# Performance work log

Hardware: AMD Instinct MI355X
Metric: run time of the kernel (lower is better)

## Reference

```python
import jax, jax.numpy as jnp
import numpy as np

H, W, C, B = 16, 16, 2048, 32
HEADS = 4
D1, D2 = 256, 128


def _build_edges(h, w):
    """Lattice + mirror + disease-node + self-loop edges (PyG GATConv default adds self loops)."""
    idx = lambda i, j: i * w + j
    edges = []
    for i in range(h):
        for j in range(w):
            if i + 1 < h:
                edges += [(idx(i, j), idx(i + 1, j)), (idx(i + 1, j), idx(i, j))]
            if j + 1 < w:
                edges += [(idx(i, j), idx(i, j + 1)), (idx(i, j + 1), idx(i, j))]
            mj = w - j - 1
            if mj != j:
                edges.append((idx(i, j), idx(i, mj)))
    n = h * w
    for i in range(n):  # disease node (index n), bidirectional
        edges += [(i, n), (n, i)]
    for i in range(n + 1):  # self loops
        edges.append((i, i))
    e = np.asarray(edges, dtype=np.int32)
    return jnp.asarray(e[:, 0]), jnp.asarray(e[:, 1])


def setup_inputs() -> dict:
    key = jax.random.key(0)
    ks = jax.random.split(key, 16)
    s = 0.02
    src, dst = _build_edges(H, W)
    return {
        "fmap": jax.random.normal(ks[0], (B, C, H, W), jnp.float32),
        "W1": jax.random.normal(ks[1], (C, HEADS * D1), jnp.float32) * s,
        "a_src1": jax.random.normal(ks[2], (HEADS, D1), jnp.float32) * s,
        "a_dst1": jax.random.normal(ks[3], (HEADS, D1), jnp.float32) * s,
        "b1": jnp.zeros((D1,), jnp.float32),
        "W2": jax.random.normal(ks[4], (D1, HEADS * D2), jnp.float32) * s,
        "a_src2": jax.random.normal(ks[5], (HEADS, D2), jnp.float32) * s,
        "a_dst2": jax.random.normal(ks[6], (HEADS, D2), jnp.float32) * s,
        "b2": jnp.zeros((D2,), jnp.float32),
        "Wp": jax.random.normal(ks[7], (D2, 1), jnp.float32) * s,
        "bp": jnp.zeros((1,), jnp.float32),
        "Wc1": jax.random.normal(ks[8], (D2, 64), jnp.float32) * s,
        "bc1": jnp.zeros((64,), jnp.float32),
        "Wc2": jax.random.normal(ks[9], (64, 1), jnp.float32) * s,
        "bc2": jnp.zeros((1,), jnp.float32),
        "src": src,
        "dst": dst,
    }


def _gat_layer(x, src, dst, Wm, a_s, a_d, b, heads, out_dim):
    """PyG GATConv math: concat=False (mean over heads), leaky_relu slope 0.2."""
    N = x.shape[0]
    h = (x @ Wm).reshape(N, heads, out_dim)           # [N, H, D]
    es = jnp.sum(h * a_s, axis=-1)                    # [N, H]
    ed = jnp.sum(h * a_d, axis=-1)                    # [N, H]
    e = jax.nn.leaky_relu(es[src] + ed[dst], 0.2)     # [E, H]
    m = jax.ops.segment_max(e, dst, num_segments=N)   # softmax over incoming edges
    alpha = jnp.exp(e - m[dst])
    denom = jax.ops.segment_sum(alpha, dst, num_segments=N)
    alpha = alpha / (denom[dst] + 1e-16)
    agg = jax.ops.segment_sum(alpha[:, :, None] * h[src], dst, num_segments=N)
    return agg.mean(axis=1) + b                       # [N, D]


def reference(fmap, W1, a_src1, a_dst1, b1, W2, a_src2, a_dst2, b2,
              Wp, bp, Wc1, bc1, Wc2, bc2, src, dst):
    Bn, Cc, Hh, Ww = fmap.shape
    nodes = fmap.reshape(Bn, Cc, Hh * Ww).transpose(0, 2, 1)   # [B, HW, C]
    nodes = jnp.concatenate([nodes, jnp.zeros((Bn, 1, Cc), nodes.dtype)], axis=1)

    def per_graph(x):
        x = _gat_layer(x, src, dst, W1, a_src1, a_dst1, b1, HEADS, D1)
        x = _gat_layer(x, src, dst, W2, a_src2, a_dst2, b2, HEADS, D2)
        w = jax.nn.sigmoid(x @ Wp + bp)               # [N, 1] attention pool weights
        g = jnp.mean(x * w, axis=0)                   # global_mean_pool, single graph
        h1 = jax.nn.relu(g @ Wc1 + bc1)
        pred = jax.nn.sigmoid(h1 @ Wc2 + bc2)         # [1]
        return pred[0], w[:, 0]

    preds, atts = jax.vmap(per_graph)(nodes)          # [B], [B, N]
    return preds, atts
```

## Files before the change

### kernel.cpp

```cpp
#include <hip/hip_runtime.h>

typedef __bf16 bf16_t;
typedef __bf16 bf16x8 __attribute__((ext_vector_type(8)));
typedef float f32x4 __attribute__((ext_vector_type(4)));

#define MPAD  8320
#define NNODE 257
#define NB    32

__device__ __forceinline__ void gld_lds16(const bf16_t* g, bf16_t* l) {
    __builtin_amdgcn_global_load_lds(
        (const __attribute__((address_space(1))) void*)g,
        (__attribute__((address_space(3))) void*)l, 16, 0, 0);
}

__global__ __launch_bounds__(256) void setup_kernel(const float* __restrict__ W1, bf16_t* __restrict__ W1t,
                                                    const float* __restrict__ W2, bf16_t* __restrict__ W2t,
                                                    const float* __restrict__ fmap, bf16_t* __restrict__ X,
                                                    const int* __restrict__ dstv, int E,
                                                    int* __restrict__ indptr, int* __restrict__ eidx,
                                                    float* __restrict__ zbase, bf16_t* __restrict__ out1) {
    __shared__ float smem[64 * 65];
    int idx = blockIdx.x, t = threadIdx.x;
    if (idx < 2176) {
        const float* W; bf16_t* Wt; int K, N, kt, nt;
        if (idx < 2048) { W = W1; Wt = W1t; K = 2048; N = 1024; kt = idx >> 5; nt = idx & 31; }
        else { int l = idx - 2048; W = W2; Wt = W2t; K = 256; N = 512; kt = l >> 4; nt = l & 15; }
        int k0 = kt * 32, n0 = nt * 32;
        int tx = t & 31, ty = t >> 5;
#pragma unroll
        for (int i = 0; i < 4; i++)
            smem[(ty + i * 8) * 33 + tx] = W[(size_t)(k0 + ty + i * 8) * N + n0 + tx];
        __syncthreads();
#pragma unroll
        for (int i = 0; i < 4; i++)
            Wt[(size_t)(n0 + ty + i * 8) * K + k0 + tx] = (bf16_t)smem[tx * 33 + ty + i * 8];
    } else if (idx < 6272) {
        int local = idx - 2176;
        int ct = local & 31, rem = local >> 5;
        int nt = rem & 3, b = rem >> 2;
        int c0 = ct * 64, n0 = nt * 64;
        const float* f = fmap + (size_t)b * 2048 * 256;
        int ln = t & 63, lc = t >> 6;
#pragma unroll
        for (int i = 0; i < 16; i++) {
            int c = lc + i * 4;
            smem[c * 65 + ln] = f[(size_t)(c0 + c) * 256 + n0 + ln];
        }
        __syncthreads();
        int sn = t >> 3, sc = (t & 7) * 8;
#pragma unroll
        for (int half = 0; half < 2; half++) {
            int n = sn + half * 32;
            bf16_t tmp[8];
#pragma unroll
            for (int j = 0; j < 8; j++) tmp[j] = (bf16_t)smem[(sc + j) * 65 + n];
            *(bf16x8*)&X[(size_t)(b * 257 + n0 + n) * 2048 + c0 + sc] = *(bf16x8*)tmp;
        }
    } else if (idx < 6402) {
        int local = idx - 6272;
        uint4* p = (uint4*)zbase + (size_t)local * 256;
        p[t] = uint4{0, 0, 0, 0};
    } else if (idx < 6530) {
        int i = idx - 6402;
        int row = (i < 32) ? (i * 257 + 256) : (8224 + (i - 32));
        uint4* p = (uint4*)(X + (size_t)row * 2048);
        p[t] = uint4{0, 0, 0, 0};
    } else if (idx < 6542) {
        int local = idx - 6530;
        uint4* p = (uint4*)((char*)(out1 + (size_t)8224 * 256) + (size_t)local * 4096);
        p[t] = uint4{0, 0, 0, 0};
    } else {
        __shared__ int cnt[258];
        __shared__ int off[258];
        for (int i = t; i < 258; i += 256) cnt[i] = 0;
        __syncthreads();
        for (int e = t; e < E; e += 256) atomicAdd(&cnt[dstv[e] + 1], 1);
        __syncthreads();
        if (t == 0) {
            int s = 0;
            for (int i = 0; i < 258; i++) { s += cnt[i]; off[i] = s; }
        }
        __syncthreads();
        for (int i = t; i < 258; i += 256) indptr[i] = off[i];
        __syncthreads();
        for (int e = t; e < E; e += 256) {
            int p = atomicAdd(&off[dstv[e]], 1);
            eidx[p] = e;
        }
    }
}

__global__ __launch_bounds__(128, 2) void gemm_kernel(const bf16_t* __restrict__ A,
                                                      const bf16_t* __restrict__ Bt,
                                                      bf16_t* __restrict__ C,
                                                      const float* __restrict__ asrc,
                                                      const float* __restrict__ adst,
                                                      float* __restrict__ es,
                                                      float* __restrict__ ed,
                                                      int K, int N, int headD) {
    __shared__ __align__(16) bf16_t sm[3 * 8192];
    int row0 = blockIdx.y * 128, col0 = blockIdx.x * 128;
    int t = threadIdx.x;
    int wave = t >> 6, lane = t & 63;
    int srow = lane >> 2, scol = (lane & 3) * 8;
    const bf16_t* Abase = A + (size_t)row0 * K;
    const bf16_t* Bbase = Bt + (size_t)col0 * K;
    f32x4 acc[4][8] = {};
    int fr = lane & 15;
    int kq = (lane >> 4) * 8;
    int nk = K >> 5;
    auto issue = [&](int kt, int stage) {
        bf16_t* As = sm + stage * 8192;
        bf16_t* Bs = As + 4096;
        int k0 = kt << 5;
#pragma unroll
        for (int c = 0; c < 4; c++) {
            int chunk = wave * 4 + c;
            int row = chunk * 16 + srow;
            gld_lds16(Abase + (size_t)row * K + k0 + scol, &As[chunk * 512]);
            gld_lds16(Bbase + (size_t)row * K + k0 + scol, &Bs[chunk * 512]);
        }
    };
    issue(0, 0);
    if (nk > 1) issue(1, 1);
    for (int k = 0; k < nk; k++) {
        int cur = k % 3;
        if (k + 2 < nk) {
            issue(k + 2, (k + 2) % 3);
            asm volatile("s_waitcnt vmcnt(16)" ::: "memory");
        } else if (k + 1 < nk) {
            asm volatile("s_waitcnt vmcnt(8)" ::: "memory");
        } else {
            asm volatile("s_waitcnt vmcnt(0)" ::: "memory");
        }
        __builtin_amdgcn_s_barrier();
        const bf16_t* As = sm + cur * 8192;
        const bf16_t* Bs = As + 4096;
        bf16x8 af[4], bfv[8];
#pragma unroll
        for (int mr = 0; mr < 4; mr++)
            af[mr] = *(const bf16x8*)&As[(wave * 64 + mr * 16 + fr) * 32 + kq];
#pragma unroll
        for (int nc = 0; nc < 8; nc++)
            bfv[nc] = *(const bf16x8*)&Bs[(nc * 16 + fr) * 32 + kq];
#pragma unroll
        for (int mr = 0; mr < 4; mr++)
#pragma unroll
            for (int nc = 0; nc < 8; nc++)
                acc[mr][nc] = __builtin_amdgcn_mfma_f32_16x16x32_bf16(
                    af[mr], bfv[nc], acc[mr][nc], 0, 0, 0);
        asm volatile("s_waitcnt lgkmcnt(0)" ::: "memory");
        __builtin_amdgcn_s_barrier();
    }
#pragma unroll
    for (int mr = 0; mr < 4; mr++) {
        int crow = row0 + wave * 64 + mr * 16 + (lane >> 4) * 4;
#pragma unroll
        for (int nc = 0; nc < 8; nc++) {
            int ccol = col0 + nc * 16 + (lane & 15);
#pragma unroll
            for (int r = 0; r < 4; r++)
                C[(size_t)(crow + r) * N + ccol] = (bf16_t)acc[mr][nc][r];
        }
    }
    int h = col0 / headD;
    float as_v[8], ad_v[8];
#pragma unroll
    for (int nc = 0; nc < 8; nc++) {
        int ccol = col0 + nc * 16 + (lane & 15);
        as_v[nc] = asrc[ccol];
        ad_v[nc] = adst[ccol];
    }
#pragma unroll
    for (int mr = 0; mr < 4; mr++)
#pragma unroll
        for (int r = 0; r < 4; r++) {
            float ps = 0.f, pd = 0.f;
#pragma unroll
            for (int nc = 0; nc < 8; nc++) {
                float v = acc[mr][nc][r];
                ps += v * as_v[nc];
                pd += v * ad_v[nc];
            }
#pragma unroll
            for (int m = 1; m < 16; m <<= 1) {
                ps += __shfl_xor(ps, m);
                pd += __shfl_xor(pd, m);
            }
            if ((lane & 15) == 0) {
                int row = row0 + wave * 64 + mr * 16 + (lane >> 4) * 4 + r;
                atomicAdd(&es[row * 4 + h], ps);
                atomicAdd(&ed[row * 4 + h], pd);
            }
        }
}

template<int D>
__global__ __launch_bounds__(256) void attn_kernel(const bf16_t* __restrict__ Hb,
                                                   const float* __restrict__ es,
                                                   const float* __restrict__ ed,
                                                   const int* __restrict__ indptr,
                                                   const int* __restrict__ eidx,
                                                   const int* __restrict__ srcv,
                                                   const float* __restrict__ bias,
                                                   float* __restrict__ outf,
                                                   bf16_t* __restrict__ outb) {
    constexpr int VPL = D / 64;
    int d = blockIdx.x, b = blockIdx.y;
    int r = b * 257 + d;
    int t = threadIdx.x, wv = t >> 6, lane = t & 63;
    int e0 = indptr[d];
    int deg = indptr[d + 1] - e0;
    __shared__ float alpha[NNODE * 4];
    __shared__ int   ssh[NNODE];
    __shared__ float wred[4][8];
    __shared__ float mh4[4], rh4[4];
    __shared__ float osh[4][D];
    const float4 edv = *(const float4*)&ed[r * 4];
    float edh[4] = {edv.x, edv.y, edv.z, edv.w};
    float lmax[4] = {-1e30f, -1e30f, -1e30f, -1e30f};
    for (int i = t; i < deg; i += 256) {
        int s = srcv[eidx[e0 + i]];
        ssh[i] = s;
        float4 e4 = *(const float4*)&es[(b * 257 + s) * 4];
        float ev[4] = {e4.x, e4.y, e4.z, e4.w};
#pragma unroll
        for (int h = 0; h < 4; h++) {
            float v = ev[h] + edh[h];
            v = v > 0.f ? v : 0.2f * v;
            alpha[i * 4 + h] = v;
            lmax[h] = fmaxf(lmax[h], v);
        }
    }
#pragma unroll
    for (int h = 0; h < 4; h++) {
        float m = lmax[h];
#pragma unroll
        for (int o = 32; o > 0; o >>= 1) m = fmaxf(m, __shfl_down(m, o));
        if (lane == 0) wred[h][wv] = m;
    }
    __syncthreads();
    if (t < 4)
        mh4[t] = fmaxf(fmaxf(wred[t][0], wred[t][1]), fmaxf(wred[t][2], wred[t][3]));
    __syncthreads();
    float lsum[4] = {0.f, 0.f, 0.f, 0.f};
    for (int i = t; i < deg; i += 256) {
#pragma unroll
        for (int h = 0; h < 4; h++) {
            float a = __expf(alpha[i * 4 + h] - mh4[h]);
            alpha[i * 4 + h] = a;
            lsum[h] += a;
        }
    }
#pragma unroll
    for (int h = 0; h < 4; h++) {
        float s = lsum[h];
#pragma unroll
        for (int o = 32; o > 0; o >>= 1) s += __shfl_down(s, o);
        if (lane == 0) wred[h][wv] = s;
    }
    __syncthreads();
    if (t < 4)
        rh4[t] = 1.f / (wred[t][0] + wred[t][1] + wred[t][2] + wred[t][3] + 1e-16f);
    __syncthreads();
    float rh = rh4[wv];
    float acc[VPL] = {};
    const bf16_t* hb = Hb + (size_t)(b * 257) * 4 * D + wv * D + lane * VPL;
    for (int i = 0; i < deg; i++) {
        float a = alpha[i * 4 + wv] * rh;
        const bf16_t* hr = hb + (size_t)ssh[i] * 4 * D;
        bf16_t xv[VPL];
        __builtin_memcpy(xv, hr, VPL * 2);
#pragma unroll
        for (int v = 0; v < VPL; v++) acc[v] += a * (float)xv[v];
    }
#pragma unroll
    for (int v = 0; v < VPL; v++) osh[wv][lane * VPL + v] = acc[v];
    __syncthreads();
    if (t < D) {
        float o = (osh[0][t] + osh[1][t] + osh[2][t] + osh[3][t]) * 0.25f + bias[t];
        if (outb) outb[(size_t)r * D + t] = (bf16_t)o;
        else      outf[(size_t)r * D + t] = o;
    }
}

__global__ __launch_bounds__(256) void head_kernel(const float* __restrict__ out2,
                                                   const float* __restrict__ Wp,
                                                   const float* __restrict__ bp,
                                                   const float* __restrict__ Wc1,
                                                   const float* __restrict__ bc1,
                                                   const float* __restrict__ Wc2,
                                                   const float* __restrict__ bc2,
                                                   float* __restrict__ outp) {
    int b = blockIdx.x, t = threadIdx.x, wv = t >> 6, lane = t & 63;
    __shared__ float wsh[NNODE];
    __shared__ float gpart[2][128];
    __shared__ float gsh[128];
    __shared__ float h1[64];
    const float* X = out2 + (size_t)b * 257 * 128;
    float wp0 = Wp[lane], wp1 = Wp[64 + lane], bp0 = bp[0];
    for (int n = wv; n < 257; n += 4) {
        const float* xr = X + n * 128;
        float s = xr[lane] * wp0 + xr[64 + lane] * wp1;
#pragma unroll
        for (int o = 32; o > 0; o >>= 1) s += __shfl_down(s, o);
        if (lane == 0) {
            float wvv = 1.f / (1.f + __expf(-(s + bp0)));
            wsh[n] = wvv;
            outp[32 + b * 257 + n] = wvv;
        }
    }
    __syncthreads();
    {
        int dim = t & 127, half = t >> 7;
        float s = 0.f;
        for (int n = half; n < 257; n += 2) s += X[n * 128 + dim] * wsh[n];
        gpart[half][dim] = s;
    }
    __syncthreads();
    if (t < 128) gsh[t] = (gpart[0][t] + gpart[1][t]) * (1.f / 257.f);
    __syncthreads();
    if (t < 64) {
        float s = bc1[t];
        for (int k = 0; k < 128; k++) s += gsh[k] * Wc1[k * 64 + t];
        h1[t] = fmaxf(s, 0.f);
    }
    __syncthreads();
    if (t == 0) {
        float s = bc2[0];
        for (int j = 0; j < 64; j++) s += h1[j] * Wc2[j];
        outp[b] = 1.f / (1.f + expf(-s));
    }
}

extern "C" void kernel_launch(void* const* d_in, const int* in_sizes, int n_in,
                              void* d_out, int out_size, void* d_ws, size_t ws_size,
                              hipStream_t stream) {
    const float* fmap   = (const float*)d_in[0];
    const float* W1     = (const float*)d_in[1];
    const float* a_src1 = (const float*)d_in[2];
    const float* a_dst1 = (const float*)d_in[3];
    const float* b1     = (const float*)d_in[4];
    const float* W2     = (const float*)d_in[5];
    const float* a_src2 = (const float*)d_in[6];
    const float* a_dst2 = (const float*)d_in[7];
    const float* b2     = (const float*)d_in[8];
    const float* Wp     = (const float*)d_in[9];
    const float* bp     = (const float*)d_in[10];
    const float* Wc1    = (const float*)d_in[11];
    const float* bc1    = (const float*)d_in[12];
    const float* Wc2    = (const float*)d_in[13];
    const float* bc2    = (const float*)d_in[14];
    const int*   srcv   = (const int*)d_in[15];
    const int*   dstv   = (const int*)d_in[16];
    int E = in_sizes[15];
    float* outp = (float*)d_out;

    char* w = (char*)d_ws;
    size_t off = 0;
    auto alloc = [&](size_t bytes) -> void* {
        void* p = w + off;
        off += (bytes + 255) & ~(size_t)255;
        return p;
    };
    bf16_t* X    = (bf16_t*)alloc((size_t)MPAD * 2048 * sizeof(bf16_t));
    bf16_t* W1t  = (bf16_t*)alloc((size_t)1024 * 2048 * sizeof(bf16_t));
    bf16_t* W2t  = (bf16_t*)alloc((size_t)512 * 256 * sizeof(bf16_t));
    bf16_t* H1   = (bf16_t*)alloc((size_t)MPAD * 1024 * sizeof(bf16_t));
    bf16_t* out1 = (bf16_t*)alloc((size_t)MPAD * 256 * sizeof(bf16_t));
    bf16_t* H2   = (bf16_t*)alloc((size_t)MPAD * 512 * sizeof(bf16_t));
    float*  out2 = (float*)alloc((size_t)MPAD * 128 * sizeof(float));
    float*  es1  = (float*)alloc((size_t)MPAD * 4 * sizeof(float));
    float*  ed1  = (float*)alloc((size_t)MPAD * 4 * sizeof(float));
    float*  es2  = (float*)alloc((size_t)MPAD * 4 * sizeof(float));
    float*  ed2  = (float*)alloc((size_t)MPAD * 4 * sizeof(float));
    int*  indptr = (int*)alloc(258 * sizeof(int));
    int*  eidx   = (int*)alloc((size_t)E * sizeof(int));

    setup_kernel<<<6543, 256, 0, stream>>>(W1, W1t, W2, W2t, fmap, X, dstv, E,
                                           indptr, eidx, es1, out1);
    gemm_kernel<<<dim3(1024 / 128, MPAD / 128), 128, 0, stream>>>(
        X, W1t, H1, a_src1, a_dst1, es1, ed1, 2048, 1024, 256);
    attn_kernel<256><<<dim3(NNODE, NB), 256, 0, stream>>>(H1, es1, ed1, indptr, eidx,
                                                          srcv, b1, nullptr, out1);
    gemm_kernel<<<dim3(512 / 128, MPAD / 128), 128, 0, stream>>>(
        out1, W2t, H2, a_src2, a_dst2, es2, ed2, 256, 512, 128);
    attn_kernel<128><<<dim3(NNODE, NB), 256, 0, stream>>>(H2, es2, ed2, indptr, eidx,
                                                          srcv, b2, out2, nullptr);
    head_kernel<<<NB, 256, 0, stream>>>(out2, Wp, bp, Wc1, bc1, Wc2, bc2, outp);

    (void)n_in; (void)out_size; (void)ws_size;
}
```

Measured before the change: 355.0 us.

## Remap GEMM tiles across XCDs with 4 waves and stage attention features in LDS

The GEMM now runs 256-thread blocks with a 2x2 wave tiling of the 128x128 tile and a 1D grid that interleaves tiles round-robin across the 8 XCDs, to improve L2 locality. The attention kernel is rewritten so each block handles one graph and one column slice: it stages that slice of H, the es/ed scores and the edge lists in LDS, then processes destination nodes one per wave, recomputing the softmax terms per edge. Setup now stores source node ids in CSR order directly, so the extra eidx indirection is gone. The new attention path gives far fewer blocks (256) and heavy LDS use, which may limit occupancy, and it relies on a fixed EMAX bound on the edge count.

```diff
diff --git a/kernel.cpp b/kernel.cpp
--- a/kernel.cpp
+++ b/kernel.cpp
@@ -1,12 +1,14 @@
 #include <hip/hip_runtime.h>
 
 typedef __bf16 bf16_t;
+typedef __bf16 bf16x2 __attribute__((ext_vector_type(2)));
 typedef __bf16 bf16x8 __attribute__((ext_vector_type(8)));
 typedef float f32x4 __attribute__((ext_vector_type(4)));
 
 #define MPAD  8320
 #define NNODE 257
 #define NB    32
+#define EMAX  2080
 
 __device__ __forceinline__ void gld_lds16(const bf16_t* g, bf16_t* l) {
     __builtin_amdgcn_global_load_lds(
@@ -17,8 +19,8 @@
 __global__ __launch_bounds__(256) void setup_kernel(const float* __restrict__ W1, bf16_t* __restrict__ W1t,
                                                     const float* __restrict__ W2, bf16_t* __restrict__ W2t,
                                                     const float* __restrict__ fmap, bf16_t* __restrict__ X,
-                                                    const int* __restrict__ dstv, int E,
-                                                    int* __restrict__ indptr, int* __restrict__ eidx,
+                                                    const int* __restrict__ srcv, const int* __restrict__ dstv,
+                                                    int E, int* __restrict__ indptr, int* __restrict__ csrc,
                                                     float* __restrict__ zbase, bf16_t* __restrict__ out1) {
     __shared__ float smem[64 * 65];
     int idx = blockIdx.x, t = threadIdx.x;
@@ -86,27 +88,34 @@
         __syncthreads();
         for (int e = t; e < E; e += 256) {
             int p = atomicAdd(&off[dstv[e]], 1);
-            eidx[p] = e;
-        }
-    }
-}
-
-__global__ __launch_bounds__(128, 2) void gemm_kernel(const bf16_t* __restrict__ A,
-                                                      const bf16_t* __restrict__ Bt,
-                                                      bf16_t* __restrict__ C,
-                                                      const float* __restrict__ asrc,
-                                                      const float* __restrict__ adst,
-                                                      float* __restrict__ es,
-                                                      float* __restrict__ ed,
-                                                      int K, int N, int headD) {
+            csrc[p] = srcv[e];
+        }
+    }
+}
+
+__global__ __launch_bounds__(256) void gemm_kernel(const bf16_t* __restrict__ A,
+                                                   const bf16_t* __restrict__ Bt,
+                                                   bf16_t* __restrict__ C,
+                                                   const float* __restrict__ asrc,
+                                                   const float* __restrict__ adst,
+                                                   float* __restrict__ es,
+                                                   float* __restrict__ ed,
+                                                   int K, int N, int hshift,
+                                                   int tiles_per_xcd, int ncol_log2, int ntiles) {
     __shared__ __align__(16) bf16_t sm[3 * 8192];
-    int row0 = blockIdx.y * 128, col0 = blockIdx.x * 128;
+    int linear = blockIdx.x;
+    int gt = (linear & 7) * tiles_per_xcd + (linear >> 3);
+    if (gt >= ntiles) return;
+    int row0 = (gt >> ncol_log2) * 128;
+    int col0 = (gt & ((1 << ncol_log2) - 1)) * 128;
     int t = threadIdx.x;
     int wave = t >> 6, lane = t & 63;
+    int wr = wave >> 1, wc = wave & 1;
+    int ch0 = wave * 2;
     int srow = lane >> 2, scol = (lane & 3) * 8;
     const bf16_t* Abase = A + (size_t)row0 * K;
     const bf16_t* Bbase = Bt + (size_t)col0 * K;
-    f32x4 acc[4][8] = {};
+    f32x4 acc[4][4] = {};
     int fr = lane & 15;
     int kq = (lane >> 4) * 8;
     int nk = K >> 5;
@@ -115,8 +124,8 @@
         bf16_t* Bs = As + 4096;
         int k0 = kt << 5;
 #pragma unroll
-        for (int c = 0; c < 4; c++) {
-            int chunk = wave * 4 + c;
+        for (int c = 0; c < 2; c++) {
+            int chunk = ch0 + c;
             int row = chunk * 16 + srow;
             gld_lds16(Abase + (size_t)row * K + k0 + scol, &As[chunk * 512]);
             gld_lds16(Bbase + (size_t)row * K + k0 + scol, &Bs[chunk * 512]);
@@ -128,26 +137,26 @@
         int cur = k % 3;
         if (k + 2 < nk) {
             issue(k + 2, (k + 2) % 3);
-            asm volatile("s_waitcnt vmcnt(16)" ::: "memory");
+            asm volatile("s_waitcnt vmcnt(8)" ::: "memory");
         } else if (k + 1 < nk) {
-            asm volatile("s_waitcnt vmcnt(8)" ::: "memory");
+            asm volatile("s_waitcnt vmcnt(4)" ::: "memory");
         } else {
             asm volatile("s_waitcnt vmcnt(0)" ::: "memory");
         }
         __builtin_amdgcn_s_barrier();
         const bf16_t* As = sm + cur * 8192;
         const bf16_t* Bs = As + 4096;
-        bf16x8 af[4], bfv[8];
+        bf16x8 af[4], bfv[4];
 #pragma unroll
         for (int mr = 0; mr < 4; mr++)
-            af[mr] = *(const bf16x8*)&As[(wave * 64 + mr * 16 + fr) * 32 + kq];
-#pragma unroll
-        for (int nc = 0; nc < 8; nc++)
-            bfv[nc] = *(const bf16x8*)&Bs[(nc * 16 + fr) * 32 + kq];
+            af[mr] = *(const bf16x8*)&As[(wr * 64 + mr * 16 + fr) * 32 + kq];
+#pragma unroll
+        for (int nc = 0; nc < 4; nc++)
+            bfv[nc] = *(const bf16x8*)&Bs[(wc * 64 + nc * 16 + fr) * 32 + kq];
 #pragma unroll
         for (int mr = 0; mr < 4; mr++)
 #pragma unroll
-            for (int nc = 0; nc < 8; nc++)
+            for (int nc = 0; nc < 4; nc++)
                 acc[mr][nc] = __builtin_amdgcn_mfma_f32_16x16x32_bf16(
                     af[mr], bfv[nc], acc[mr][nc], 0, 0, 0);
         asm volatile("s_waitcnt lgkmcnt(0)" ::: "memory");
@@ -155,20 +164,20 @@
     }
 #pragma unroll
     for (int mr = 0; mr < 4; mr++) {
-        int crow = row0 + wave * 64 + mr * 16 + (lane >> 4) * 4;
-#pragma unroll
-        for (int nc = 0; nc < 8; nc++) {
-            int ccol = col0 + nc * 16 + (lane & 15);
+        int crow = row0 + wr * 64 + mr * 16 + (lane >> 4) * 4;
+#pragma unroll
+        for (int nc = 0; nc < 4; nc++) {
+            int ccol = col0 + wc * 64 + nc * 16 + (lane & 15);
 #pragma unroll
             for (int r = 0; r < 4; r++)
                 C[(size_t)(crow + r) * N + ccol] = (bf16_t)acc[mr][nc][r];
         }
     }
-    int h = col0 / headD;
-    float as_v[8], ad_v[8];
-#pragma unroll
-    for (int nc = 0; nc < 8; nc++) {
-        int ccol = col0 + nc * 16 + (lane & 15);
+    int h = (col0 + wc * 64) >> hshift;
+    float as_v[4], ad_v[4];
+#pragma unroll
+    for (int nc = 0; nc < 4; nc++) {
+        int ccol = col0 + wc * 64 + nc * 16 + (lane & 15);
         as_v[nc] = asrc[ccol];
         ad_v[nc] = adst[ccol];
     }
@@ -178,7 +187,7 @@
         for (int r = 0; r < 4; r++) {
             float ps = 0.f, pd = 0.f;
 #pragma unroll
-            for (int nc = 0; nc < 8; nc++) {
+            for (int nc = 0; nc < 4; nc++) {
                 float v = acc[mr][nc][r];
                 ps += v * as_v[nc];
                 pd += v * ad_v[nc];
@@ -189,99 +198,99 @@
                 pd += __shfl_xor(pd, m);
             }
             if ((lane & 15) == 0) {
-                int row = row0 + wave * 64 + mr * 16 + (lane >> 4) * 4 + r;
+                int row = row0 + wr * 64 + mr * 16 + (lane >> 4) * 4 + r;
                 atomicAdd(&es[row * 4 + h], ps);
                 atomicAdd(&ed[row * 4 + h], pd);
             }
         }
 }
 
-template<int D>
+template<int D, int R>
 __global__ __launch_bounds__(256) void attn_kernel(const bf16_t* __restrict__ Hb,
                                                    const float* __restrict__ es,
                                                    const float* __restrict__ ed,
                                                    const int* __restrict__ indptr,
-                                                   const int* __restrict__ eidx,
-                                                   const int* __restrict__ srcv,
+                                                   const int* __restrict__ csrc,
                                                    const float* __restrict__ bias,
                                                    float* __restrict__ outf,
-                                                   bf16_t* __restrict__ outb) {
-    constexpr int VPL = D / 64;
-    int d = blockIdx.x, b = blockIdx.y;
-    int r = b * 257 + d;
+                                                   bf16_t* __restrict__ outb, int E) {
+    constexpr int W = 4 * D;
+    constexpr int NP = R / 2;
+    constexpr int CPN = R / 2;
+    __shared__ bf16_t Hl[257 * 4 * R];
+    __shared__ float  esl[257 * 4];
+    __shared__ float  edl[257 * 4];
+    __shared__ int    csl[EMAX];
+    __shared__ int    ipl[258];
+    int b = blockIdx.x, q = blockIdx.y;
     int t = threadIdx.x, wv = t >> 6, lane = t & 63;
-    int e0 = indptr[d];
-    int deg = indptr[d + 1] - e0;
-    __shared__ float alpha[NNODE * 4];
-    __shared__ int   ssh[NNODE];
-    __shared__ float wred[4][8];
-    __shared__ float mh4[4], rh4[4];
-    __shared__ float osh[4][D];
-    const float4 edv = *(const float4*)&ed[r * 4];
-    float edh[4] = {edv.x, edv.y, edv.z, edv.w};
-    float lmax[4] = {-1e30f, -1e30f, -1e30f, -1e30f};
-    for (int i = t; i < deg; i += 256) {
-        int s = srcv[eidx[e0 + i]];
-        ssh[i] = s;
-        float4 e4 = *(const float4*)&es[(b * 257 + s) * 4];
-        float ev[4] = {e4.x, e4.y, e4.z, e4.w};
-#pragma unroll
-        for (int h = 0; h < 4; h++) {
-            float v = ev[h] + edh[h];
+    const bf16_t* Hg = Hb + (size_t)(b * 257) * W + q * R;
+    for (int idx = t; idx < 257 * CPN; idx += 256) {
+        int n = idx / CPN, rem = idx - n * CPN;
+        int h = rem / (R / 8), c = rem - h * (R / 8);
+        bf16x8 v = *(const bf16x8*)(Hg + (size_t)n * W + h * D + c * 8);
+        *(bf16x8*)&Hl[(n * 4 + h) * R + c * 8] = v;
+    }
+    for (int idx = t; idx < 257; idx += 256) {
+        *(float4*)&esl[idx * 4] = *(const float4*)(es + (size_t)(b * 257 + idx) * 4);
+        *(float4*)&edl[idx * 4] = *(const float4*)(ed + (size_t)(b * 257 + idx) * 4);
+    }
+    for (int i = t; i < E; i += 256) csl[i] = csrc[i];
+    for (int i = t; i < 258; i += 256) ipl[i] = indptr[i];
+    __syncthreads();
+    int h2 = lane >> 4, jp = lane & 15;
+    for (int d = wv; d < 257; d += 4) {
+        int e0 = ipl[d], e1 = ipl[d + 1], deg = e1 - e0;
+        int hh = lane & 3;
+        float edh = edl[d * 4 + hh];
+        float vmax = -1e30f;
+        for (int i = (lane >> 2); i < deg; i += 16) {
+            int s = csl[e0 + i];
+            float v = esl[s * 4 + hh] + edh;
             v = v > 0.f ? v : 0.2f * v;
-            alpha[i * 4 + h] = v;
-            lmax[h] = fmaxf(lmax[h], v);
-        }
-    }
-#pragma unroll
-    for (int h = 0; h < 4; h++) {
-        float m = lmax[h];
-#pragma unroll
-        for (int o = 32; o > 0; o >>= 1) m = fmaxf(m, __shfl_down(m, o));
-        if (lane == 0) wred[h][wv] = m;
-    }
-    __syncthreads();
-    if (t < 4)
-        mh4[t] = fmaxf(fmaxf(wred[t][0], wred[t][1]), fmaxf(wred[t][2], wred[t][3]));
-    __syncthreads();
-    float lsum[4] = {0.f, 0.f, 0.f, 0.f};
-    for (int i = t; i < deg; i += 256) {
-#pragma unroll
-        for (int h = 0; h < 4; h++) {
-            float a = __expf(alpha[i * 4 + h] - mh4[h]);
-            alpha[i * 4 + h] = a;
-            lsum[h] += a;
-        }
-    }
-#pragma unroll
-    for (int h = 0; h < 4; h++) {
-        float s = lsum[h];
-#pragma unroll
-        for (int o = 32; o > 0; o >>= 1) s += __shfl_down(s, o);
-        if (lane == 0) wred[h][wv] = s;
-    }
-    __syncthreads();
-    if (t < 4)
-        rh4[t] = 1.f / (wred[t][0] + wred[t][1] + wred[t][2] + wred[t][3] + 1e-16f);
-    __syncthreads();
-    float rh = rh4[wv];
-    float acc[VPL] = {};
-    const bf16_t* hb = Hb + (size_t)(b * 257) * 4 * D + wv * D + lane * VPL;
-    for (int i = 0; i < deg; i++) {
-        float a = alpha[i * 4 + wv] * rh;
-        const bf16_t* hr = hb + (size_t)ssh[i] * 4 * D;
-        bf16_t xv[VPL];
-        __builtin_memcpy(xv, hr, VPL * 2);
-#pragma unroll
-        for (int v = 0; v < VPL; v++) acc[v] += a * (float)xv[v];
-    }
-#pragma unroll
-    for (int v = 0; v < VPL; v++) osh[wv][lane * VPL + v] = acc[v];
-    __syncthreads();
-    if (t < D) {
-        float o = (osh[0][t] + osh[1][t] + osh[2][t] + osh[3][t]) * 0.25f + bias[t];
-        if (outb) outb[(size_t)r * D + t] = (bf16_t)o;
-        else      outf[(size_t)r * D + t] = o;
+            vmax = fmaxf(vmax, v);
+        }
+#pragma unroll
+        for (int mk = 4; mk < 64; mk <<= 1) vmax = fmaxf(vmax, __shfl_xor(vmax, mk));
+        float vsum = 0.f;
+        for (int i = (lane >> 2); i < deg; i += 16) {
+            int s = csl[e0 + i];
+            float v = esl[s * 4 + hh] + edh;
+            v = v > 0.f ? v : 0.2f * v;
+            vsum += __expf(v - vmax);
+        }
+#pragma unroll
+        for (int mk = 4; mk < 64; mk <<= 1) vsum += __shfl_xor(vsum, mk);
+        float rinv = 1.f / (vsum + 1e-16f);
+        float mm = __shfl(vmax, h2);
+        float rr = __shfl(rinv, h2);
+        float edc = edl[d * 4 + h2];
+        float ax = 0.f, ay = 0.f;
+#pragma unroll 2
+        for (int i = e0; i < e1; i++) {
+            int s = csl[i];
+            float v = esl[s * 4 + h2] + edc;
+            v = v > 0.f ? v : 0.2f * v;
+            float a = __expf(v - mm) * rr;
+            bf16x2 xv = *(const bf16x2*)&Hl[(s * 4 + h2) * R + jp * 2];
+            ax += a * (float)xv[0];
+            ay += a * (float)xv[1];
+        }
+        ax += __shfl_xor(ax, 16); ax += __shfl_xor(ax, 32);
+        ay += __shfl_xor(ay, 16); ay += __shfl_xor(ay, 32);
+        if (lane < NP) {
+            int col = q * R + jp * 2;
+            size_t row = (size_t)(b * 257 + d);
+            float o0 = ax * 0.25f + bias[col];
+            float o1 = ay * 0.25f + bias[col + 1];
+            if (outb) {
+                outb[row * D + col]     = (bf16_t)o0;
+                outb[row * D + col + 1] = (bf16_t)o1;
+            } else {
+                outf[row * D + col]     = o0;
+                outf[row * D + col + 1] = o1;
+            }
+        }
     }
 }
 
@@ -376,18 +385,18 @@
     float*  es2  = (float*)alloc((size_t)MPAD * 4 * sizeof(float));
     float*  ed2  = (float*)alloc((size_t)MPAD * 4 * sizeof(float));
     int*  indptr = (int*)alloc(258 * sizeof(int));
-    int*  eidx   = (int*)alloc((size_t)E * sizeof(int));
-
-    setup_kernel<<<6543, 256, 0, stream>>>(W1, W1t, W2, W2t, fmap, X, dstv, E,
-                                           indptr, eidx, es1, out1);
-    gemm_kernel<<<dim3(1024 / 128, MPAD / 128), 128, 0, stream>>>(
-        X, W1t, H1, a_src1, a_dst1, es1, ed1, 2048, 1024, 256);
-    attn_kernel<256><<<dim3(NNODE, NB), 256, 0, stream>>>(H1, es1, ed1, indptr, eidx,
-                                                          srcv, b1, nullptr, out1);
-    gemm_kernel<<<dim3(512 / 128, MPAD / 128), 128, 0, stream>>>(
-        out1, W2t, H2, a_src2, a_dst2, es2, ed2, 256, 512, 128);
-    attn_kernel<128><<<dim3(NNODE, NB), 256, 0, stream>>>(H2, es2, ed2, indptr, eidx,
-                                                          srcv, b2, out2, nullptr);
+    int*  csrc   = (int*)alloc((size_t)E * sizeof(int));
+
+    setup_kernel<<<6543, 256, 0, stream>>>(W1, W1t, W2, W2t, fmap, X, srcv, dstv, E,
+                                           indptr, csrc, es1, out1);
+    gemm_kernel<<<520, 256, 0, stream>>>(
+        X, W1t, H1, a_src1, a_dst1, es1, ed1, 2048, 1024, 8, 65, 3, 520);
+    attn_kernel<256, 32><<<dim3(NB, 8), 256, 0, stream>>>(
+        H1, es1, ed1, indptr, csrc, b1, nullptr, out1, E);
+    gemm_kernel<<<264, 256, 0, stream>>>(
+        out1, W2t, H2, a_src2, a_dst2, es2, ed2, 256, 512, 7, 33, 2, 260);
+    attn_kernel<128, 16><<<dim3(NB, 8), 256, 0, stream>>>(
+        H2, es2, ed2, indptr, csrc, b2, out2, nullptr, E);
     head_kernel<<<NB, 256, 0, stream>>>(out2, Wp, bp, Wc1, bc1, Wc2, bc2, outp);
 
     (void)n_in; (void)out_size; (void)ws_size;
```

Result: slower. 494.9 us (+39.4%).
